# Optimization experiments

Measured on AMD Instinct MI355X. Metric: run time of the kernel, lower is better.

The kernel has to match this reference:

```python
import jax, jax.numpy as jnp
import numpy as np

B = 2; QD = 128; H = QD; W = QD; NQ = QD * QD
EMBED = 256; HEADS = 8; POINTS = 4; D = EMBED // HEADS; FFN = 512


def setup_inputs() -> dict:
    key = jax.random.key(0)
    ks = jax.random.split(key, 16)
    s = 0.02
    rn = lambda k, shp: jax.random.normal(k, shp, jnp.float32) * s
    return {
        'q': jax.random.normal(ks[0], (B, NQ, EMBED), jnp.float32),
        'W_off': rn(ks[1], (EMBED, HEADS * POINTS * 2)),
        'b_off': rn(ks[2], (HEADS * POINTS * 2,)),
        'W_attn': rn(ks[3], (EMBED, HEADS * POINTS)),
        'b_attn': rn(ks[4], (HEADS * POINTS,)),
        'W_val': rn(ks[5], (EMBED, EMBED)),
        'b_val': rn(ks[6], (EMBED,)),
        'W_out': rn(ks[7], (EMBED, EMBED)),
        'b_out': rn(ks[8], (EMBED,)),
        'W1': rn(ks[9], (EMBED, FFN)),
        'b1': rn(ks[10], (FFN,)),
        'W2': rn(ks[11], (FFN, EMBED)),
        'b2': rn(ks[12], (EMBED,)),
        'gamma': jnp.ones((EMBED,), jnp.float32),
        'beta': jnp.zeros((EMBED,), jnp.float32),
    }


def _layernorm(x, g, b):
    m = x.mean(-1, keepdims=True)
    v = ((x - m) ** 2).mean(-1, keepdims=True)
    return (x - m) * jax.lax.rsqrt(v + 1e-5) * g + b


def _msda(q, W_off, b_off, W_attn, b_attn, W_val, b_val, W_out, b_out):
    # value projection; value == query here. (B, NQ, EMBED)
    value = q @ W_val + b_val
    v = value.reshape(B, NQ, HEADS, D).transpose(0, 2, 1, 3)  # (B, heads, Nv, D)

    off = (q @ W_off + b_off).reshape(B, NQ, HEADS, POINTS, 2)
    aw = jax.nn.softmax((q @ W_attn + b_attn).reshape(B, NQ, HEADS, POINTS), axis=-1)

    # reference points: torch.meshgrid(linspace, linspace, indexing='xy')
    lin = jnp.linspace(0.0, 1.0, QD)
    gx, gy = jnp.meshgrid(lin, lin, indexing='xy')
    ref = jnp.stack([gx, gy], -1).reshape(1, NQ, 1, 1, 2)

    # offset_normalizer = [W, H]; sampling locations in [0,1]
    loc = ref + off / jnp.array([W, H], jnp.float32)
    # grid_sample bilinear, align_corners=False: pixel = loc * size - 0.5
    px = (loc[..., 0] * W - 0.5).transpose(0, 2, 1, 3)  # (B, heads, NQ, P)
    py = (loc[..., 1] * H - 0.5).transpose(0, 2, 1, 3)

    x0 = jnp.floor(px)
    y0 = jnp.floor(py)
    sampled = jnp.zeros((B, HEADS, NQ, POINTS, D), jnp.float32)
    for dy in (0.0, 1.0):
        for dx in (0.0, 1.0):
            xi = x0 + dx
            yi = y0 + dy
            wgt = (1.0 - jnp.abs(px - xi)) * (1.0 - jnp.abs(py - yi))
            valid = ((xi >= 0) & (xi <= W - 1) & (yi >= 0) & (yi <= H - 1)).astype(jnp.float32)
            idx = (jnp.clip(yi, 0, H - 1).astype(jnp.int32) * W
                   + jnp.clip(xi, 0, W - 1).astype(jnp.int32))  # (B, heads, NQ, P)
            g = jnp.take_along_axis(v, idx.reshape(B, HEADS, NQ * POINTS, 1), axis=2)
            g = g.reshape(B, HEADS, NQ, POINTS, D)
            sampled = sampled + g * (wgt * valid)[..., None]

    awt = aw.transpose(0, 2, 1, 3)  # (B, heads, NQ, P)
    out = (sampled * awt[..., None]).sum(3)  # (B, heads, NQ, D)
    out = out.transpose(0, 2, 1, 3).reshape(B, NQ, EMBED)
    # mmcv: dropout(output_proj(out)) + identity ; dropout is identity at eval
    return out @ W_out + b_out + q


def reference(q, W_off, b_off, W_attn, b_attn, W_val, b_val, W_out, b_out,
              W1, b1, W2, b2, gamma, beta):
    attn = _msda(q, W_off, b_off, W_attn, b_attn, W_val, b_val, W_out, b_out)
    x = attn + q  # outer residual in the module (in addition to mmcv's internal one)
    ffn = _layernorm(jax.nn.relu(x @ W1 + b1) @ W2 + b2, gamma, beta)
    return x + ffn
```

## Files before the change

kernel.cpp:

```cpp
#include <hip/hip_runtime.h>
#include <hip/hip_bf16.h>
#include <cstddef>
#include <cstdint>

#define B_      2
#define QD_     128
#define NQ_     (QD_ * QD_)
#define EMBED_  256
#define HEADS_  8
#define POINTS_ 4
#define FFN_    512
#define RTOT_   (B_ * NQ_)
#define NCATP_  384

using bf16x8 = __attribute__((ext_vector_type(8))) short;
using f32x4  = __attribute__((ext_vector_type(4))) float;

__device__ __forceinline__ short f2bf(float f) {
    unsigned u = __float_as_uint(f);
    u += 0x7FFFu + ((u >> 16) & 1u);
    return (short)(u >> 16);
}
__device__ __forceinline__ float bf2f(short s) {
    return __uint_as_float(((unsigned)(unsigned short)s) << 16);
}

#define GLDS(gp, lp) __builtin_amdgcn_global_load_lds( \
        (const __attribute__((address_space(1))) void*)(gp), \
        (__attribute__((address_space(3))) void*)(lp), 16, 0, 0)

#define WCAT_ELEMS  (NCATP_ * 256)
#define WOUT_ELEMS  (256 * 256)
#define W1_ELEMS    (512 * 256)
#define W2_ELEMS    (256 * 512)
#define PREP_TOTAL  (WCAT_ELEMS + WOUT_ELEMS + W1_ELEMS + W2_ELEMS)
#define CVT_BLOCKS  (RTOT_ * EMBED_ / 8 / 256)
#define PREP_BLOCKS ((PREP_TOTAL + 255) / 256)

__global__ __launch_bounds__(256) void prep_all(
        const float* __restrict__ q, short* __restrict__ qbf,
        const float* __restrict__ Wv, const float* __restrict__ Wo,
        const float* __restrict__ Wa, const float* __restrict__ bv,
        const float* __restrict__ bo, const float* __restrict__ ba,
        const float* __restrict__ W_out, const float* __restrict__ W1,
        const float* __restrict__ W2,
        short* __restrict__ WcatT, short* __restrict__ WoutT,
        short* __restrict__ W1T, short* __restrict__ W2T,
        float* __restrict__ bcat) {
    const int b = blockIdx.x;
    if (b < CVT_BLOCKS) {
        const size_t i = (size_t)b * 256 + threadIdx.x;
        const float4 f0 = *(const float4*)(q + i * 8);
        const float4 f1 = *(const float4*)(q + i * 8 + 4);
        bf16x8 v;
        v[0] = f2bf(f0.x); v[1] = f2bf(f0.y); v[2] = f2bf(f0.z); v[3] = f2bf(f0.w);
        v[4] = f2bf(f1.x); v[5] = f2bf(f1.y); v[6] = f2bf(f1.z); v[7] = f2bf(f1.w);
        *(bf16x8*)(qbf + i * 8) = v;
        return;
    }
    int idx = (b - CVT_BLOCKS) * 256 + threadIdx.x;
    if (idx < WCAT_ELEMS) {
        int c = idx >> 8, k = idx & 255;
        float v = 0.f;
        if (c < 256)      v = Wv[k * 256 + c];
        else if (c < 320) v = Wo[k * 64 + (c - 256)];
        else if (c < 352) v = Wa[k * 32 + (c - 320)];
        WcatT[idx] = f2bf(v);
    } else if (idx < WCAT_ELEMS + WOUT_ELEMS) {
        int j = idx - WCAT_ELEMS; int c = j >> 8, k = j & 255;
        WoutT[j] = f2bf(W_out[k * 256 + c]);
    } else if (idx < WCAT_ELEMS + WOUT_ELEMS + W1_ELEMS) {
        int j = idx - (WCAT_ELEMS + WOUT_ELEMS); int c = j >> 8, k = j & 255;
        W1T[j] = f2bf(W1[k * 512 + c]);
    } else if (idx < PREP_TOTAL) {
        int j = idx - (WCAT_ELEMS + WOUT_ELEMS + W1_ELEMS); int c = j >> 9, k = j & 511;
        W2T[j] = f2bf(W2[k * 256 + c]);
    }
    if (idx < NCATP_) {
        float v = 0.f;
        if (idx < 256)      v = bv[idx];
        else if (idx < 320) v = bo[idx - 256];
        else if (idx < 352) v = ba[idx - 320];
        bcat[idx] = v;
    }
}

enum { EP_SPLIT = 3 };

template <int EP>
__global__ __launch_bounds__(256) void gemm_mfma(
        const short* __restrict__ A,
        const short* __restrict__ Bt,
        const float* __restrict__ bias,
        float* __restrict__ Cf,
        short* __restrict__ Cb,
        int M, int N, int K) {
    __shared__ __align__(16) short As[2][128 * 64];
    __shared__ __align__(16) short Bs[2][128 * 64];

    const int t    = threadIdx.x;
    const int ln   = t & 63;
    const int w    = t >> 6;
    const int wr   = w >> 1;
    const int wc   = w & 1;
    const int lrow = ln & 15;
    const int lkg  = ln >> 4;

    const int gx   = gridDim.x;
    const int nwg  = gx * gridDim.y;
    const int flat = blockIdx.y * gx + blockIdx.x;
    const int q8   = nwg >> 3;
    const int swz  = (flat & 7) * q8 + (flat >> 3);
    const int row0 = (swz / gx) * 128;
    const int col0 = (swz % gx) * 128;

    f32x4 acc[4][4] = {};

    auto stage = [&](int buf, int k0) {
        #pragma unroll
        for (int j = 0; j < 4; ++j) {
            const int c0 = (w * 4 + j) * 64;
            const int c  = c0 + ln;
            const int r  = c >> 3;
            const int s  = (c & 7) ^ (r & 7);
            GLDS(A  + (size_t)(row0 + r) * K + (k0 + s * 8), &As[buf][c0 * 8]);
            GLDS(Bt + (size_t)(col0 + r) * K + (k0 + s * 8), &Bs[buf][c0 * 8]);
        }
    };

    stage(0, 0);
    __syncthreads();
    int cur = 0;
    for (int k0 = 0; k0 < K; k0 += 64) {
        if (k0 + 64 < K) stage(cur ^ 1, k0 + 64);
        #pragma unroll
        for (int ks = 0; ks < 2; ++ks) {
            const int slot = ((ks * 4 + lkg) ^ (lrow & 7)) * 8;
            bf16x8 af[4], bfr[4];
            #pragma unroll
            for (int m = 0; m < 4; ++m)
                af[m] = *(const bf16x8*)&As[cur][(wr * 64 + m * 16 + lrow) * 64 + slot];
            #pragma unroll
            for (int n = 0; n < 4; ++n)
                bfr[n] = *(const bf16x8*)&Bs[cur][(wc * 64 + n * 16 + lrow) * 64 + slot];
            #pragma unroll
            for (int m = 0; m < 4; ++m)
                #pragma unroll
                for (int n = 0; n < 4; ++n)
                    acc[m][n] = __builtin_amdgcn_mfma_f32_16x16x32_bf16(
                        af[m], bfr[n], acc[m][n], 0, 0, 0);
        }
        __syncthreads();
        cur ^= 1;
    }

    const int orow = (ln >> 4) * 4;
    const int ocol = ln & 15;
    #pragma unroll
    for (int m = 0; m < 4; ++m) {
        #pragma unroll
        for (int n = 0; n < 4; ++n) {
            const int col = col0 + wc * 64 + n * 16 + ocol;
            const float bv = bias[col];
            #pragma unroll
            for (int rr = 0; rr < 4; ++rr) {
                const int row = row0 + wr * 64 + m * 16 + orow + rr;
                float v = acc[m][n][rr] + bv;
                if (col < 256) Cb[(size_t)row * 256 + col] = f2bf(v);
                else           Cf[(size_t)row * 128 + (col - 256)] = v;
            }
        }
    }
}

__global__ __launch_bounds__(512) void gemm_x_ffn1(
        const short* __restrict__ msda,
        const short* __restrict__ WoutT,
        const float* __restrict__ b_out,
        const short* __restrict__ qbf,
        const short* __restrict__ W1T,
        const float* __restrict__ b1,
        short* __restrict__ xbf,
        short* __restrict__ hid) {
    __shared__ __align__(16) short xs[128 * 256];
    __shared__ __align__(16) short stg[128 * 192];
    short* As = stg;
    short* Bs = stg + 128 * 64;

    const int t    = threadIdx.x;
    const int ln   = t & 63;
    const int w    = t >> 6;
    const int wr   = w >> 2;
    const int wc   = w & 3;
    const int lrow = ln & 15;
    const int lkg  = ln >> 4;
    const int row0 = blockIdx.x * 128;
    const int orow = lkg * 4;
    const int ocol = lrow;

    f32x4 acc[4][4] = {};
    for (int kt = 0; kt < 4; ++kt) {
        #pragma unroll
        for (int j = 0; j < 2; ++j) {
            const int c0 = (w * 2 + j) * 64;
            const int cc = c0 + ln;
            const int r  = cc >> 3;
            const int s  = (cc & 7) ^ (r & 7);
            GLDS(msda + (size_t)(row0 + r) * 256 + kt * 64 + s * 8, &As[c0 * 8]);
        }
        #pragma unroll
        for (int j = 0; j < 4; ++j) {
            const int c0 = (w * 4 + j) * 64;
            const int cc = c0 + ln;
            const int r  = cc >> 3;
            const int s  = (cc & 7) ^ (r & 7);
            GLDS(WoutT + (size_t)r * 256 + kt * 64 + s * 8, &Bs[c0 * 8]);
        }
        __syncthreads();
        #pragma unroll
        for (int ks = 0; ks < 2; ++ks) {
            const int slot = ((ks * 4 + lkg) ^ (lrow & 7)) * 8;
            bf16x8 af[4], bfr[4];
            #pragma unroll
            for (int m = 0; m < 4; ++m)
                af[m] = *(const bf16x8*)&As[(wr * 64 + m * 16 + lrow) * 64 + slot];
            #pragma unroll
            for (int n = 0; n < 4; ++n)
                bfr[n] = *(const bf16x8*)&Bs[(wc * 64 + n * 16 + lrow) * 64 + slot];
            #pragma unroll
            for (int m = 0; m < 4; ++m)
                #pragma unroll
                for (int n = 0; n < 4; ++n)
                    acc[m][n] = __builtin_amdgcn_mfma_f32_16x16x32_bf16(
                        af[m], bfr[n], acc[m][n], 0, 0, 0);
        }
        __syncthreads();
    }

    #pragma unroll
    for (int m = 0; m < 4; ++m) {
        #pragma unroll
        for (int n = 0; n < 4; ++n) {
            const int kk  = n * 16 + ocol;
            const int col = wc * 64 + kk;
            const float bv = b_out[col];
            #pragma unroll
            for (int rr = 0; rr < 4; ++rr) {
                const int row = wr * 64 + m * 16 + orow + rr;
                float v = acc[m][n][rr] + bv
                        + 2.f * bf2f(qbf[(size_t)(row0 + row) * 256 + col]);
                const short bb = f2bf(v);
                xbf[(size_t)(row0 + row) * 256 + col] = bb;
                xs[wc * 8192 + row * 64 + ((kk >> 3) ^ (row & 7)) * 8 + (kk & 7)] = bb;
            }
        }
    }
    __syncthreads();

    #pragma unroll 1
    for (int p = 0; p < 2; ++p) {
        f32x4 acc2[4][4] = {};
        for (int kt = 0; kt < 4; ++kt) {
            #pragma unroll
            for (int j = 0; j < 4; ++j) {
                const int c0 = (w * 4 + j) * 64;
                const int cc = c0 + ln;
                const int r  = cc >> 3;
                const int s  = (cc & 7) ^ (r & 7);
                GLDS(W1T + (size_t)(p * 256 + r) * 256 + kt * 64 + s * 8, &Bs[c0 * 8]);
            }
            __syncthreads();
            #pragma unroll
            for (int ks = 0; ks < 2; ++ks) {
                const int slot = ((ks * 4 + lkg) ^ (lrow & 7)) * 8;
                bf16x8 af[4], bfr[4];
                #pragma unroll
                for (int m = 0; m < 4; ++m)
                    af[m] = *(const bf16x8*)&xs[kt * 8192 + (wr * 64 + m * 16 + lrow) * 64 + slot];
                #pragma unroll
                for (int n = 0; n < 4; ++n)
                    bfr[n] = *(const bf16x8*)&Bs[(wc * 64 + n * 16 + lrow) * 64 + slot];
                #pragma unroll
                for (int m = 0; m < 4; ++m)
                    #pragma unroll
                    for (int n = 0; n < 4; ++n)
                        acc2[m][n] = __builtin_amdgcn_mfma_f32_16x16x32_bf16(
                            af[m], bfr[n], acc2[m][n], 0, 0, 0);
            }
            __syncthreads();
        }
        #pragma unroll
        for (int m = 0; m < 4; ++m) {
            #pragma unroll
            for (int n = 0; n < 4; ++n) {
                const int col = p * 256 + wc * 64 + n * 16 + ocol;
                const float bv = b1[col];
                #pragma unroll
                for (int rr = 0; rr < 4; ++rr) {
                    const int row = wr * 64 + m * 16 + orow + rr;
                    hid[(size_t)(row0 + row) * 512 + col] =
                        f2bf(fmaxf(acc2[m][n][rr] + bv, 0.f));
                }
            }
        }
    }
}

__global__ __launch_bounds__(256) void gemm_ln(
        const short* __restrict__ A,
        const short* __restrict__ Bt,
        const float* __restrict__ bias,
        const short* __restrict__ xres,
        const float* __restrict__ gamma, const float* __restrict__ beta,
        float* __restrict__ out, int M, int K) {
    __shared__ __align__(16) short As[2][64 * 64];
    __shared__ __align__(16) short Bs[256 * 64];
    __shared__ float red[64][4][2];

    const int t    = threadIdx.x;
    const int ln   = t & 63;
    const int w    = t >> 6;
    const int lrow = ln & 15;
    const int lkg  = ln >> 4;
    const int row0 = blockIdx.x * 64;

    f32x4 acc[4][4] = {};

    auto stage_a = [&](int buf, int k0) {
        #pragma unroll
        for (int j = 0; j < 2; ++j) {
            const int c0 = (w * 2 + j) * 64;
            const int c  = c0 + ln;
            const int r  = c >> 3;
            const int s  = (c & 7) ^ (r & 7);
            GLDS(A + (size_t)(row0 + r) * K + (k0 + s * 8), &As[buf][c0 * 8]);
        }
    };
    auto stage_b = [&](int k0) {
        #pragma unroll
        for (int j = 0; j < 8; ++j) {
            const int c0 = (w * 8 + j) * 64;
            const int c  = c0 + ln;
            const int r  = c >> 3;
            const int s  = (c & 7) ^ (r & 7);
            GLDS(Bt + (size_t)r * K + (k0 + s * 8), &Bs[c0 * 8]);
        }
    };

    stage_a(0, 0);
    stage_b(0);
    __syncthreads();
    int buf = 0;
    for (int kt = 0; kt < 8; ++kt) {
        if (kt < 7) stage_a(buf ^ 1, kt * 64 + 64);
        #pragma unroll
        for (int ks = 0; ks < 2; ++ks) {
            const int slot = ((ks * 4 + lkg) ^ (lrow & 7)) * 8;
            bf16x8 af[4], bfr[4];
            #pragma unroll
            for (int m = 0; m < 4; ++m)
                af[m] = *(const bf16x8*)&As[buf][(m * 16 + lrow) * 64 + slot];
            #pragma unroll
            for (int n = 0; n < 4; ++n)
                bfr[n] = *(const bf16x8*)&Bs[(w * 64 + n * 16 + lrow) * 64 + slot];
            #pragma unroll
            for (int m = 0; m < 4; ++m)
                #pragma unroll
                for (int n = 0; n < 4; ++n)
                    acc[m][n] = __builtin_amdgcn_mfma_f32_16x16x32_bf16(
                        af[m], bfr[n], acc[m][n], 0, 0, 0);
        }
        __syncthreads();
        if (kt < 7) {
            stage_b(kt * 64 + 64);
            __syncthreads();
        }
        buf ^= 1;
    }

    const int orow = lkg * 4;
    const int ocol = lrow;

    #pragma unroll
    for (int n = 0; n < 4; ++n) {
        const float bv = bias[w * 64 + n * 16 + ocol];
        #pragma unroll
        for (int m = 0; m < 4; ++m)
            #pragma unroll
            for (int rr = 0; rr < 4; ++rr)
                acc[m][n][rr] += bv;
    }

    #pragma unroll
    for (int m = 0; m < 4; ++m) {
        #pragma unroll
        for (int rr = 0; rr < 4; ++rr) {
            float s = 0.f, sq = 0.f;
            #pragma unroll
            for (int n = 0; n < 4; ++n) {
                const float v = acc[m][n][rr];
                s += v; sq += v * v;
            }
            #pragma unroll
            for (int o = 1; o < 16; o <<= 1) {
                s  += __shfl_xor(s, o, 64);
                sq += __shfl_xor(sq, o, 64);
            }
            if (ocol == 0) {
                const int row = m * 16 + orow + rr;
                red[row][w][0] = s;
                red[row][w][1] = sq;
            }
        }
    }
    __syncthreads();

    #pragma unroll
    for (int m = 0; m < 4; ++m) {
        #pragma unroll
        for (int rr = 0; rr < 4; ++rr) {
            const int row = m * 16 + orow + rr;
            const float S  = red[row][0][0] + red[row][1][0] + red[row][2][0] + red[row][3][0];
            const float SQ = red[row][0][1] + red[row][1][1] + red[row][2][1] + red[row][3][1];
            const float mean = S * (1.0f / 256.0f);
            const float var  = SQ * (1.0f / 256.0f) - mean * mean;
            const float rs   = rsqrtf(var + 1e-5f);
            const size_t rbase = (size_t)(row0 + row) * 256;
            #pragma unroll
            for (int n = 0; n < 4; ++n) {
                const int col = w * 64 + n * 16 + ocol;
                out[rbase + col] = bf2f(xres[rbase + col])
                                 + (acc[m][n][rr] - mean) * rs * gamma[col] + beta[col];
            }
        }
    }
}

__global__ __launch_bounds__(256) void msda_sample(
        const float* __restrict__ pm, const short* __restrict__ vcomp,
        short* __restrict__ msda) {
    __shared__ int   s_off[8][32][4];
    __shared__ float s_c[8][32][4];

    const int t  = threadIdx.x;
    const int r0 = blockIdx.x * 8;
    const int bq = r0 >> 14;

    {
        const int g = t >> 5, cmb = t & 31, h = cmb >> 2, p = cmb & 3;
        const int r = r0 + g;
        const int n = r & (NQ_ - 1);
        const int gi = n >> 7, gj = n & 127;
        const float* pr = pm + (size_t)r * 128;

        const float l0 = pr[64 + h * 4 + 0], l1 = pr[64 + h * 4 + 1];
        const float l2 = pr[64 + h * 4 + 2], l3 = pr[64 + h * 4 + 3];
        const float mx = fmaxf(fmaxf(l0, l1), fmaxf(l2, l3));
        const float sum = expf(l0 - mx) + expf(l1 - mx) + expf(l2 - mx) + expf(l3 - mx);
        const float lp = pr[64 + h * 4 + p];
        const float aw = expf(lp - mx) / sum;

        const float ox = pr[h * 8 + p * 2 + 0];
        const float oy = pr[h * 8 + p * 2 + 1];
        const float px = (gj * (1.0f / 127.0f) + ox * (1.0f / 128.0f)) * 128.0f - 0.5f;
        const float py = (gi * (1.0f / 127.0f) + oy * (1.0f / 128.0f)) * 128.0f - 0.5f;
        const float x0f = floorf(px), y0f = floorf(py);
        const int   x0 = (int)x0f, y0 = (int)y0f;
        const float fx = px - x0f, fy = py - y0f;
        const int x0c = min(max(x0, 0), 127), x1c = min(max(x0 + 1, 0), 127);
        const int y0c = min(max(y0, 0), 127), y1c = min(max(y0 + 1, 0), 127);
        const float vx0 = ((unsigned)x0 <= 127u) ? 1.f : 0.f;
        const float vx1 = ((unsigned)(x0 + 1) <= 127u) ? 1.f : 0.f;
        const float vy0 = ((unsigned)y0 <= 127u) ? 1.f : 0.f;
        const float vy1 = ((unsigned)(y0 + 1) <= 127u) ? 1.f : 0.f;

        s_off[g][cmb][0] = (y0c * 128 + x0c) * 512;
        s_off[g][cmb][1] = (y0c * 128 + x1c) * 512;
        s_off[g][cmb][2] = (y1c * 128 + x0c) * 512;
        s_off[g][cmb][3] = (y1c * 128 + x1c) * 512;
        s_c[g][cmb][0] = aw * (1.f - fx) * (1.f - fy) * vx0 * vy0;
        s_c[g][cmb][1] = aw * fx * (1.f - fy) * vx1 * vy0;
        s_c[g][cmb][2] = aw * (1.f - fx) * fy * vx0 * vy1;
        s_c[g][cmb][3] = aw * fx * fy * vx1 * vy1;
    }
    __syncthreads();

    const int half = t >> 7;
    const int h    = (t >> 4) & 7;
    const int dd   = t & 15;
    const char* vb = (const char*)vcomp + ((size_t)bq * NQ_ * 256 + h * 32 + dd * 2) * 2;

    #pragma unroll
    for (int it = 0; it < 4; ++it) {
        const int g = it * 2 + half;
        float a0 = 0.f, a1 = 0.f;
        #pragma unroll
        for (int p = 0; p < 4; ++p) {
            const int cmb = h * 4 + p;
            #pragma unroll
            for (int k = 0; k < 4; ++k) {
                const unsigned u = *(const unsigned*)(vb + s_off[g][cmb][k]);
                const float c = s_c[g][cmb][k];
                a0 += c * __uint_as_float(u << 16);
                a1 += c * __uint_as_float(u & 0xffff0000u);
            }
        }
        const int r = r0 + g;
        const unsigned o = (unsigned)(unsigned short)f2bf(a0)
                         | ((unsigned)(unsigned short)f2bf(a1) << 16);
        *(unsigned*)&msda[(size_t)r * 256 + h * 32 + dd * 2] = o;
    }
}

extern "C" void kernel_launch(void* const* d_in, const int* in_sizes, int n_in,
                              void* d_out, int out_size, void* d_ws, size_t ws_size,
                              hipStream_t stream) {
    const float* q      = (const float*)d_in[0];
    const float* b_out  = (const float*)d_in[8];
    const float* b1     = (const float*)d_in[10];
    const float* b2     = (const float*)d_in[12];
    const float* gamma  = (const float*)d_in[13];
    const float* beta   = (const float*)d_in[14];

    float* out = (float*)d_out;

    char* w = (char*)d_ws;
    float* pm    = (float*)w; w += (size_t)RTOT_ * 128 * 4;
    short* vcomp = (short*)w; w += (size_t)RTOT_ * 256 * 2;
    short* qbf   = (short*)w; w += (size_t)RTOT_ * EMBED_ * 2;
    short* msda  = (short*)w; w += (size_t)RTOT_ * EMBED_ * 2;
    short* xbf   = (short*)w; w += (size_t)RTOT_ * EMBED_ * 2;
    short* hid   = (short*)w; w += (size_t)RTOT_ * FFN_ * 2;
    short* WcatT = (short*)w; w += WCAT_ELEMS * 2;
    short* WoutT = (short*)w; w += WOUT_ELEMS * 2;
    short* W1T   = (short*)w; w += W1_ELEMS * 2;
    short* W2T   = (short*)w; w += W2_ELEMS * 2;
    float* bcat  = (float*)w; w += NCATP_ * 4;

    prep_all<<<CVT_BLOCKS + PREP_BLOCKS, 256, 0, stream>>>(
        q, qbf,
        (const float*)d_in[5], (const float*)d_in[1], (const float*)d_in[3],
        (const float*)d_in[6], (const float*)d_in[2], (const float*)d_in[4],
        (const float*)d_in[7], (const float*)d_in[9], (const float*)d_in[11],
        WcatT, WoutT, W1T, W2T, bcat);

    gemm_mfma<EP_SPLIT><<<dim3(NCATP_ / 128, RTOT_ / 128), 256, 0, stream>>>(
        qbf, WcatT, bcat, pm, vcomp, RTOT_, NCATP_, EMBED_);

    msda_sample<<<RTOT_ / 8, 256, 0, stream>>>(pm, vcomp, msda);

    gemm_x_ffn1<<<RTOT_ / 128, 512, 0, stream>>>(
        msda, WoutT, b_out, qbf, W1T, b1, xbf, hid);

    gemm_ln<<<RTOT_ / 64, 256, 0, stream>>>(
        hid, W2T, b2, xbf, gamma, beta, out, RTOT_, FFN_);
}
```

Measured before the change: 103.3 us.

## Fuse q bf16 conversion into first projection GEMM with resident A tile

The fp32-to-bf16 conversion of q moves out of the prep kernel and into the first GEMM. Each 512-thread block loads a full 128x256 row slab of q, converts it, writes qbf for later use, and keeps the slab in LDS. It then loops over the three 128-column output panels, streaming only the weight tiles through a double buffer. This avoids re-reading the bf16 A operand from global memory once per column block and removes a separate pass over q. The cost is fewer, larger blocks (256 instead of 768), a serial loop over N inside each block, and more LDS per block.

New measurement: 101.1 us. 1.02x faster.

```diff
diff --git a/kernel.cpp b/kernel.cpp
--- a/kernel.cpp
+++ b/kernel.cpp
@@ -34,11 +34,9 @@
 #define W1_ELEMS    (512 * 256)
 #define W2_ELEMS    (256 * 512)
 #define PREP_TOTAL  (WCAT_ELEMS + WOUT_ELEMS + W1_ELEMS + W2_ELEMS)
-#define CVT_BLOCKS  (RTOT_ * EMBED_ / 8 / 256)
 #define PREP_BLOCKS ((PREP_TOTAL + 255) / 256)
 
-__global__ __launch_bounds__(256) void prep_all(
-        const float* __restrict__ q, short* __restrict__ qbf,
+__global__ __launch_bounds__(256) void prep_weights(
         const float* __restrict__ Wv, const float* __restrict__ Wo,
         const float* __restrict__ Wa, const float* __restrict__ bv,
         const float* __restrict__ bo, const float* __restrict__ ba,
@@ -47,18 +45,7 @@
         short* __restrict__ WcatT, short* __restrict__ WoutT,
         short* __restrict__ W1T, short* __restrict__ W2T,
         float* __restrict__ bcat) {
-    const int b = blockIdx.x;
-    if (b < CVT_BLOCKS) {
-        const size_t i = (size_t)b * 256 + threadIdx.x;
-        const float4 f0 = *(const float4*)(q + i * 8);
-        const float4 f1 = *(const float4*)(q + i * 8 + 4);
-        bf16x8 v;
-        v[0] = f2bf(f0.x); v[1] = f2bf(f0.y); v[2] = f2bf(f0.z); v[3] = f2bf(f0.w);
-        v[4] = f2bf(f1.x); v[5] = f2bf(f1.y); v[6] = f2bf(f1.z); v[7] = f2bf(f1.w);
-        *(bf16x8*)(qbf + i * 8) = v;
-        return;
-    }
-    int idx = (b - CVT_BLOCKS) * 256 + threadIdx.x;
+    int idx = blockIdx.x * 256 + threadIdx.x;
     if (idx < WCAT_ELEMS) {
         int c = idx >> 8, k = idx & 255;
         float v = 0.f;
@@ -85,91 +72,110 @@
     }
 }
 
-enum { EP_SPLIT = 3 };
-
-template <int EP>
-__global__ __launch_bounds__(256) void gemm_mfma(
-        const short* __restrict__ A,
-        const short* __restrict__ Bt,
-        const float* __restrict__ bias,
-        float* __restrict__ Cf,
-        short* __restrict__ Cb,
-        int M, int N, int K) {
-    __shared__ __align__(16) short As[2][128 * 64];
+__global__ __launch_bounds__(512) void gemm1_fused(
+        const float* __restrict__ q,
+        const short* __restrict__ WcatT,
+        const float* __restrict__ bcat,
+        short* __restrict__ qbf,
+        short* __restrict__ vcomp,
+        float* __restrict__ pm) {
+    __shared__ __align__(16) short xs[128 * 256];
     __shared__ __align__(16) short Bs[2][128 * 64];
 
     const int t    = threadIdx.x;
     const int ln   = t & 63;
     const int w    = t >> 6;
-    const int wr   = w >> 1;
-    const int wc   = w & 1;
+    const int wr   = w >> 2;
+    const int wc   = w & 3;
     const int lrow = ln & 15;
     const int lkg  = ln >> 4;
-
-    const int gx   = gridDim.x;
-    const int nwg  = gx * gridDim.y;
-    const int flat = blockIdx.y * gx + blockIdx.x;
-    const int q8   = nwg >> 3;
-    const int swz  = (flat & 7) * q8 + (flat >> 3);
-    const int row0 = (swz / gx) * 128;
-    const int col0 = (swz % gx) * 128;
-
-    f32x4 acc[4][4] = {};
-
-    auto stage = [&](int buf, int k0) {
-        #pragma unroll
-        for (int j = 0; j < 4; ++j) {
-            const int c0 = (w * 4 + j) * 64;
+    const int row0 = blockIdx.x * 128;
+    const int orow = lkg * 4;
+    const int ocol = lrow;
+
+    auto stage_b = [&](int step, int buf) {
+        const int p  = step >> 2;
+        const int kt = step & 3;
+        #pragma unroll
+        for (int j = 0; j < 2; ++j) {
+            const int c0 = (w * 2 + j) * 64;
             const int c  = c0 + ln;
             const int r  = c >> 3;
             const int s  = (c & 7) ^ (r & 7);
-            GLDS(A  + (size_t)(row0 + r) * K + (k0 + s * 8), &As[buf][c0 * 8]);
-            GLDS(Bt + (size_t)(col0 + r) * K + (k0 + s * 8), &Bs[buf][c0 * 8]);
+            GLDS(WcatT + (size_t)(p * 128 + r) * 256 + kt * 64 + s * 8,
+                 &Bs[buf][c0 * 8]);
         }
     };
 
-    stage(0, 0);
+    stage_b(0, 0);
+    #pragma unroll
+    for (int j = 0; j < 8; ++j) {
+        const int c = t + 512 * j;
+        const int r = c >> 5;
+        const int s = c & 31;
+        const float* qp = q + (size_t)(row0 + r) * 256 + s * 8;
+        const float4 f0 = *(const float4*)qp;
+        const float4 f1 = *(const float4*)(qp + 4);
+        bf16x8 v;
+        v[0] = f2bf(f0.x); v[1] = f2bf(f0.y); v[2] = f2bf(f0.z); v[3] = f2bf(f0.w);
+        v[4] = f2bf(f1.x); v[5] = f2bf(f1.y); v[6] = f2bf(f1.z); v[7] = f2bf(f1.w);
+        *(bf16x8*)&qbf[(size_t)(row0 + r) * 256 + s * 8] = v;
+        const int kt = s >> 3, sc = s & 7;
+        *(bf16x8*)&xs[kt * 8192 + r * 64 + (sc ^ (r & 7)) * 8] = v;
+    }
     __syncthreads();
-    int cur = 0;
-    for (int k0 = 0; k0 < K; k0 += 64) {
-        if (k0 + 64 < K) stage(cur ^ 1, k0 + 64);
+
+    f32x4 acc[4][2] = {};
+    const f32x4 zero = {0.f, 0.f, 0.f, 0.f};
+
+    int buf = 0;
+    #pragma unroll 1
+    for (int step = 0; step < 12; ++step) {
+        if (step < 11) stage_b(step + 1, buf ^ 1);
+        const int kt = step & 3;
         #pragma unroll
         for (int ks = 0; ks < 2; ++ks) {
             const int slot = ((ks * 4 + lkg) ^ (lrow & 7)) * 8;
-            bf16x8 af[4], bfr[4];
+            bf16x8 af[4], bfr[2];
             #pragma unroll
             for (int m = 0; m < 4; ++m)
-                af[m] = *(const bf16x8*)&As[cur][(wr * 64 + m * 16 + lrow) * 64 + slot];
-            #pragma unroll
-            for (int n = 0; n < 4; ++n)
-                bfr[n] = *(const bf16x8*)&Bs[cur][(wc * 64 + n * 16 + lrow) * 64 + slot];
+                af[m] = *(const bf16x8*)&xs[kt * 8192 + (wr * 64 + m * 16 + lrow) * 64 + slot];
+            #pragma unroll
+            for (int n = 0; n < 2; ++n)
+                bfr[n] = *(const bf16x8*)&Bs[buf][(wc * 32 + n * 16 + lrow) * 64 + slot];
             #pragma unroll
             for (int m = 0; m < 4; ++m)
                 #pragma unroll
-                for (int n = 0; n < 4; ++n)
+                for (int n = 0; n < 2; ++n)
                     acc[m][n] = __builtin_amdgcn_mfma_f32_16x16x32_bf16(
                         af[m], bfr[n], acc[m][n], 0, 0, 0);
         }
         __syncthreads();
-        cur ^= 1;
-    }
-
-    const int orow = (ln >> 4) * 4;
-    const int ocol = ln & 15;
-    #pragma unroll
-    for (int m = 0; m < 4; ++m) {
-        #pragma unroll
-        for (int n = 0; n < 4; ++n) {
-            const int col = col0 + wc * 64 + n * 16 + ocol;
-            const float bv = bias[col];
-            #pragma unroll
-            for (int rr = 0; rr < 4; ++rr) {
-                const int row = row0 + wr * 64 + m * 16 + orow + rr;
-                float v = acc[m][n][rr] + bv;
-                if (col < 256) Cb[(size_t)row * 256 + col] = f2bf(v);
-                else           Cf[(size_t)row * 128 + (col - 256)] = v;
-            }
-        }
+        if ((step & 3) == 3) {
+            const int p = step >> 2;
+            #pragma unroll
+            for (int m = 0; m < 4; ++m) {
+                #pragma unroll
+                for (int n = 0; n < 2; ++n) {
+                    const int gcol = p * 128 + wc * 32 + n * 16 + ocol;
+                    const float bv = bcat[gcol];
+                    #pragma unroll
+                    for (int rr = 0; rr < 4; ++rr) {
+                        const int row = wr * 64 + m * 16 + orow + rr;
+                        const float v = acc[m][n][rr] + bv;
+                        if (gcol < 256) {
+                            vcomp[(size_t)(row0 + row) * 256 + gcol] = f2bf(v);
+                        } else {
+                            const int cc = gcol - 256;
+                            if (cc < 96)
+                                pm[(size_t)(row0 + row) * 128 + cc] = v;
+                        }
+                    }
+                    acc[m][n] = zero;
+                }
+            }
+        }
+        buf ^= 1;
     }
 }
 
@@ -537,15 +543,14 @@
     short* W2T   = (short*)w; w += W2_ELEMS * 2;
     float* bcat  = (float*)w; w += NCATP_ * 4;
 
-    prep_all<<<CVT_BLOCKS + PREP_BLOCKS, 256, 0, stream>>>(
-        q, qbf,
+    prep_weights<<<PREP_BLOCKS, 256, 0, stream>>>(
         (const float*)d_in[5], (const float*)d_in[1], (const float*)d_in[3],
         (const float*)d_in[6], (const float*)d_in[2], (const float*)d_in[4],
         (const float*)d_in[7], (const float*)d_in[9], (const float*)d_in[11],
         WcatT, WoutT, W1T, W2T, bcat);
 
-    gemm_mfma<EP_SPLIT><<<dim3(NCATP_ / 128, RTOT_ / 128), 256, 0, stream>>>(
-        qbf, WcatT, bcat, pm, vcomp, RTOT_, NCATP_, EMBED_);
+    gemm1_fused<<<RTOT_ / 128, 512, 0, stream>>>(
+        q, WcatT, bcat, qbf, vcomp, pm);
 
     msda_sample<<<RTOT_ / 8, 256, 0, stream>>>(pm, vcomp, msda);
 
```
